# Kernel optimization log

Measured on AMD Instinct MI355X. Metric: run time of the kernel, lower is better.

Reference implementation:

```python
import jax, jax.numpy as jnp
import numpy as np

N_NODES = 10000
IN_CH = 512
HID = 128
HEADS = 4
OUT_CH = 256
N_EDGES = 160000
NEG_SLOPE = 0.2  # PyG GATConv default


def gat_conv(x, src, dst, W, a_src, a_dst, b):
    """PyG-style GATConv. x:[N,F_in], W:[F_in,H*C], a_src/a_dst:[H,C], b:[H*C].
    src/dst already include self-loops. Returns [N, H*C] (concat heads)."""
    N = x.shape[0]
    H, C = a_src.shape
    h = (x @ W).reshape(N, H, C)                     # [N,H,C]
    e_src = jnp.einsum('nhc,hc->nh', h, a_src)        # [N,H]
    e_dst = jnp.einsum('nhc,hc->nh', h, a_dst)
    alpha = jax.nn.leaky_relu(e_src[src] + e_dst[dst], NEG_SLOPE)  # [E,H]
    # softmax over incoming edges of each destination node
    m = jax.ops.segment_max(alpha, dst, num_segments=N)            # [N,H]
    ex = jnp.exp(alpha - m[dst])
    denom = jax.ops.segment_sum(ex, dst, num_segments=N)           # [N,H]
    coeff = ex / (denom[dst] + 1e-16)                              # [E,H]
    out = jax.ops.segment_sum(coeff[:, :, None] * h[src], dst, num_segments=N)  # [N,H,C]
    return out.reshape(N, H * C) + b


def _edges_with_self_loops(edge_index, n):
    loops = jnp.arange(n, dtype=edge_index.dtype)
    src = jnp.concatenate([edge_index[0], loops])
    dst = jnp.concatenate([edge_index[1], loops])
    return src, dst


def setup_inputs() -> dict:
    key = jax.random.key(0)
    ks = jax.random.split(key, 20)
    s = 0.05
    inp = {
        'x': jax.random.normal(ks[0], (N_NODES, IN_CH), jnp.float32),
        'W1': jax.random.normal(ks[1], (IN_CH, HEADS * HID), jnp.float32) * s,
        'a1s': jax.random.normal(ks[2], (HEADS, HID), jnp.float32) * s,
        'a1d': jax.random.normal(ks[3], (HEADS, HID), jnp.float32) * s,
        'b1': jnp.zeros((HEADS * HID,), jnp.float32),
        'W2': jax.random.normal(ks[4], (HEADS * HID, HEADS * HID), jnp.float32) * s,
        'a2s': jax.random.normal(ks[5], (HEADS, HID), jnp.float32) * s,
        'a2d': jax.random.normal(ks[6], (HEADS, HID), jnp.float32) * s,
        'b2': jnp.zeros((HEADS * HID,), jnp.float32),
        'W3': jax.random.normal(ks[7], (HEADS * HID, HID), jnp.float32) * s,
        'a3s': jax.random.normal(ks[8], (1, HID), jnp.float32) * s,
        'a3d': jax.random.normal(ks[9], (1, HID), jnp.float32) * s,
        'b3': jnp.zeros((HID,), jnp.float32),
        'Wl': jax.random.normal(ks[10], (HID, OUT_CH), jnp.float32) * s,
        'bl': jnp.zeros((OUT_CH,), jnp.float32),
        'Wr': jax.random.normal(ks[11], (IN_CH, OUT_CH), jnp.float32) * s,
        'br': jnp.zeros((OUT_CH,), jnp.float32),
        'edge_index': jax.random.randint(ks[12], (2, N_EDGES), 0, N_NODES, jnp.int64 if jax.config.jax_enable_x64 else jnp.int32),
    }
    return inp


def reference(x, W1, a1s, a1d, b1, W2, a2s, a2d, b2, W3, a3s, a3d, b3, Wl, bl, Wr, br, edge_index):
    src, dst = _edges_with_self_loops(edge_index, x.shape[0])
    residual = x @ Wr + br
    h = jax.nn.elu(gat_conv(x, src, dst, W1, a1s, a1d, b1))
    h = jax.nn.elu(gat_conv(h, src, dst, W2, a2s, a2d, b2))
    h = jax.nn.elu(gat_conv(h, src, dst, W3, a3s, a3d, b3))
    return h @ Wl + bl + residual
```

## Files before the change

### kernel.cpp

```cpp
#include <hip/hip_runtime.h>
#include <hip/hip_bf16.h>
#include <cstdint>
#include <cstddef>

#define N_NODES 10000
#define M_PAD   10240
#define HEADS   4

typedef __bf16 bfrag8 __attribute__((ext_vector_type(8)));
typedef __bf16 bfrag2 __attribute__((ext_vector_type(2)));
typedef float  floatx4 __attribute__((ext_vector_type(4)));
typedef float  floatx2 __attribute__((ext_vector_type(2)));

#define S0V (M_PAD * 512 / 8)
#define S1E (512 * 512 / 8)
#define S2E (512 * 512 / 8)
#define S3E (512 * 128 / 8)
#define S4E (128 * 256 / 8)
#define S5E (512 * 256 / 8)

__global__ __launch_bounds__(256) void prep(const float* __restrict__ x,
                                            const float* __restrict__ W1,
                                            const float* __restrict__ W2,
                                            const float* __restrict__ W3,
                                            const float* __restrict__ Wl,
                                            const float* __restrict__ Wr,
                                            const int* __restrict__ edst, int E,
                                            __bf16* __restrict__ xb,
                                            __bf16* __restrict__ W1T,
                                            __bf16* __restrict__ W2T,
                                            __bf16* __restrict__ W3T,
                                            __bf16* __restrict__ WlT,
                                            __bf16* __restrict__ WrT,
                                            int* __restrict__ deg) {
    int i = blockIdx.x * 256 + threadIdx.x;
    if (i < S0V) {
        int base = i * 8;
        int row = base >> 9;
        bfrag8 r = {};
        if (row < N_NODES) {
            float4 f0 = ((const float4*)x)[i * 2];
            float4 f1 = ((const float4*)x)[i * 2 + 1];
            r[0] = (__bf16)f0.x; r[1] = (__bf16)f0.y; r[2] = (__bf16)f0.z; r[3] = (__bf16)f0.w;
            r[4] = (__bf16)f1.x; r[5] = (__bf16)f1.y; r[6] = (__bf16)f1.z; r[7] = (__bf16)f1.w;
        }
        *(bfrag8*)(xb + base) = r;
    } else if ((i -= S0V) < S1E) {
        int n = i & 511, kb = (i >> 9) * 8;
        bfrag8 r;
#pragma unroll
        for (int t = 0; t < 8; ++t) r[t] = (__bf16)W1[(kb + t) * 512 + n];
        *(bfrag8*)(W1T + n * 512 + kb) = r;
    } else if ((i -= S1E) < S2E) {
        int n = i & 511, kb = (i >> 9) * 8;
        bfrag8 r;
#pragma unroll
        for (int t = 0; t < 8; ++t) r[t] = (__bf16)W2[(kb + t) * 512 + n];
        *(bfrag8*)(W2T + n * 512 + kb) = r;
    } else if ((i -= S2E) < S3E) {
        int n = i & 127, kb = (i >> 7) * 8;
        bfrag8 r;
#pragma unroll
        for (int t = 0; t < 8; ++t) r[t] = (__bf16)W3[(kb + t) * 128 + n];
        *(bfrag8*)(W3T + n * 512 + kb) = r;
    } else if ((i -= S3E) < S4E) {
        int n = i & 255, kb = (i >> 8) * 8;
        bfrag8 r;
#pragma unroll
        for (int t = 0; t < 8; ++t) r[t] = (__bf16)Wl[(kb + t) * 256 + n];
        *(bfrag8*)(WlT + n * 128 + kb) = r;
    } else if ((i -= S4E) < S5E) {
        int n = i & 255, kb = (i >> 8) * 8;
        bfrag8 r;
#pragma unroll
        for (int t = 0; t < 8; ++t) r[t] = (__bf16)Wr[(kb + t) * 256 + n];
        *(bfrag8*)(WrT + n * 512 + kb) = r;
    } else if ((i -= S5E) < E) {
        atomicAdd(&deg[edst[i]], 1);
    }
}


__global__ __launch_bounds__(1024) void scan_kernel(const int* __restrict__ deg,
                                                    int* __restrict__ rowptr,
                                                    int* __restrict__ cursor, int n) {
    __shared__ int wtot[16], woff[16];
    int t = threadIdx.x, lane = t & 63, wv = t >> 6;
    int chunk = (n + 1023) / 1024;
    int beg = t * chunk, end = beg + chunk; if (end > n) end = n; if (beg > n) beg = n;
    int s = 0;
    for (int i = beg; i < end; ++i) s += deg[i] + 1;
    int v = s;
#pragma unroll
    for (int off = 1; off < 64; off <<= 1) {
        int o = __shfl_up(v, off);
        if (lane >= off) v += o;
    }
    if (lane == 63) wtot[wv] = v;
    __syncthreads();
    if (t == 0) {
        int r = 0;
#pragma unroll
        for (int i = 0; i < 16; ++i) { woff[i] = r; r += wtot[i]; }
        rowptr[n] = r;
    }
    __syncthreads();
    int off = woff[wv] + v - s;
    for (int i = beg; i < end; ++i) {
        rowptr[i] = off; cursor[i] = off;
        off += deg[i] + 1;
    }
}

__global__ __launch_bounds__(256) void scatter_kernel(const int* __restrict__ src,
                                                      const int* __restrict__ dst, int E, int n,
                                                      int* __restrict__ cursor,
                                                      int* __restrict__ csr) {
    int i = blockIdx.x * 256 + threadIdx.x;
    if (i < E) {
        int pos = atomicAdd(&cursor[dst[i]], 1);
        csr[pos] = src[i];
    } else if (i < E + n) {
        int v = i - E;
        int pos = atomicAdd(&cursor[v], 1);
        csr[pos] = v;
    }
}


template <int NT>
__device__ __forceinline__ void gemm_loop(const __bf16* __restrict__ A,
                                          const __bf16* __restrict__ BT, int K,
                                          int m0, int n0, int wave, int lane,
                                          __bf16* As, __bf16* Bs,
                                          floatx4 (&acc)[2][NT]) {
    int r = wave * 8 + (lane >> 3);
    int kof = (lane & 7) * 8;
    const __bf16* gA = A + (size_t)(m0 + r) * K + kof;
    const __bf16* gB = BT + (size_t)(n0 + r) * K + kof;
    __bf16* lA = As + r * 64 + kof;
    __bf16* lB = Bs + r * 64 + kof;
    const __bf16* fA = As + (wave * 32 + (lane & 15)) * 64 + (lane >> 4) * 8;
    const __bf16* fB = Bs + (lane & 15) * 64 + (lane >> 4) * 8;

    for (int k0 = 0; k0 < K; k0 += 64) {
#pragma unroll
        for (int u = 0; u < 4; ++u)
            __builtin_amdgcn_global_load_lds(
                (const __attribute__((address_space(1))) void*)(gA + (size_t)u * 32 * K),
                (__attribute__((address_space(3))) void*)(lA + u * 32 * 64), 16, 0, 0);
#pragma unroll
        for (int u = 0; u < NT / 2; ++u)
            __builtin_amdgcn_global_load_lds(
                (const __attribute__((address_space(1))) void*)(gB + (size_t)u * 32 * K),
                (__attribute__((address_space(3))) void*)(lB + u * 32 * 64), 16, 0, 0);
        gA += 64; gB += 64;
        __syncthreads();

#pragma unroll
        for (int ks = 0; ks < 2; ++ks) {
            bfrag8 a0 = *(const bfrag8*)(fA + ks * 32);
            bfrag8 a1 = *(const bfrag8*)(fA + 16 * 64 + ks * 32);
#pragma unroll
            for (int nt = 0; nt < NT; ++nt) {
                bfrag8 b = *(const bfrag8*)(fB + nt * 16 * 64 + ks * 32);
                acc[0][nt] = __builtin_amdgcn_mfma_f32_16x16x32_bf16(a0, b, acc[0][nt], 0, 0, 0);
                acc[1][nt] = __builtin_amdgcn_mfma_f32_16x16x32_bf16(a1, b, acc[1][nt], 0, 0, 0);
            }
        }
        __syncthreads();
    }
}

__global__ __launch_bounds__(256) void gemm_h(const __bf16* __restrict__ A,
                                              const __bf16* __restrict__ BT,
                                              unsigned char* __restrict__ C8,
                                              int N, int K, int H,
                                              const float* __restrict__ as_,
                                              const float* __restrict__ ad_,
                                              float* __restrict__ esp,
                                              float* __restrict__ edp) {
    __shared__ __align__(16) __bf16 As[128 * 64];
    __shared__ __align__(16) __bf16 Bs[128 * 64];
    int tid = threadIdx.x, wave = tid >> 6, lane = tid & 63;
    int m0 = blockIdx.x * 128, n0 = blockIdx.y * 128;
    floatx4 acc[2][8] = {};
    gemm_loop<8>(A, BT, K, m0, n0, wave, lane, As, Bs, acc);

    int crow = m0 + wave * 32 + (lane >> 4) * 4;
    int ccol = n0 + (lane & 15);
#pragma unroll
    for (int mt = 0; mt < 2; ++mt)
#pragma unroll
        for (int nt = 0; nt < 8; ++nt)
#pragma unroll
            for (int r = 0; r < 4; ++r) {
                float v = acc[mt][nt][r];
                size_t o = (size_t)(crow + mt * 16 + r) * N + ccol + nt * 16;
                int p = __builtin_amdgcn_cvt_pk_fp8_f32(v, v, 0, false);
                C8[o] = (unsigned char)(p & 0xff);
            }

    int head = n0 >> 7;
    float a_sv[8], a_dv[8];
#pragma unroll
    for (int nt = 0; nt < 8; ++nt) {
        int cin = nt * 16 + (lane & 15);
        a_sv[nt] = as_[head * 128 + cin];
        a_dv[nt] = ad_[head * 128 + cin];
    }
#pragma unroll
    for (int mt = 0; mt < 2; ++mt)
#pragma unroll
        for (int r = 0; r < 4; ++r) {
            float ps = 0.f, pd = 0.f;
#pragma unroll
            for (int nt = 0; nt < 8; ++nt) {
                float v = acc[mt][nt][r];
                ps += v * a_sv[nt];
                pd += v * a_dv[nt];
            }
#pragma unroll
            for (int off = 8; off; off >>= 1) {
                ps += __shfl_xor(ps, off);
                pd += __shfl_xor(pd, off);
            }
            if ((lane & 15) == 0) {
                int row = crow + mt * 16 + r;
                esp[row * H + head] = ps;
                edp[row * H + head] = pd;
            }
        }
}

__global__ __launch_bounds__(256) void gemm_final(const __bf16* __restrict__ A1,
                                                  const __bf16* __restrict__ B1T, int K1,
                                                  const __bf16* __restrict__ A2,
                                                  const __bf16* __restrict__ B2T, int K2,
                                                  float* __restrict__ C,
                                                  const float* __restrict__ bias1,
                                                  const float* __restrict__ bias2,
                                                  int M, int N) {
    __shared__ __align__(16) __bf16 As[128 * 64];
    __shared__ __align__(16) __bf16 Bs[64 * 64];
    int tid = threadIdx.x, wave = tid >> 6, lane = tid & 63;
    int m0 = blockIdx.x * 128, n0 = blockIdx.y * 64;
    floatx4 acc[2][4] = {};
    gemm_loop<4>(A1, B1T, K1, m0, n0, wave, lane, As, Bs, acc);
    gemm_loop<4>(A2, B2T, K2, m0, n0, wave, lane, As, Bs, acc);

    int crow = m0 + wave * 32 + (lane >> 4) * 4;
    int ccol = n0 + (lane & 15);
#pragma unroll
    for (int mt = 0; mt < 2; ++mt)
#pragma unroll
        for (int nt = 0; nt < 4; ++nt)
#pragma unroll
            for (int r = 0; r < 4; ++r) {
                int row = crow + mt * 16 + r;
                int col = ccol + nt * 16;
                if (row < M)
                    C[(size_t)row * N + col] = acc[mt][nt][r] + bias1[col] + bias2[col];
            }
}


template <int H>
__global__ __launch_bounds__(256) void gather_agg(const unsigned char* __restrict__ H8,
                                                  const float* __restrict__ esp,
                                                  const float* __restrict__ edp,
                                                  const int* __restrict__ rowptr,
                                                  const int* __restrict__ csr,
                                                  const float* __restrict__ bias,
                                                  __bf16* __restrict__ outb) {
    constexpr int F = H * 128;
    constexpr int CH = F / 64;
    __shared__ int   sIdx[4][64];
    __shared__ float sWgt[4][64 * H];
    int wave = threadIdx.x >> 6, lane = threadIdx.x & 63;
    int node = blockIdx.x * 4 + wave;
    if (node >= M_PAD) return;
    __bf16* op = outb + (size_t)node * F + lane * CH;
    if (node >= N_NODES) {
        if (H == 4) { bfrag8 z = {}; *(bfrag8*)op = z; }
        else        { bfrag2 z = {}; *(bfrag2*)op = z; }
        return;
    }
    int hsel = (H == 4) ? (lane >> 4) : 0;
    const unsigned char* hp = H8 + lane * CH;
    int beg = rowptr[node], end = rowptr[node + 1];
    float acc[CH] = {};
    float wsum = 0.f;

    float edv0 = 0.f, edv1 = 0.f, edv2 = 0.f, edv3 = 0.f;
    if (H == 4) {
        float4 e4 = *(const float4*)(edp + node * 4);
        edv0 = e4.x; edv1 = e4.y; edv2 = e4.z; edv3 = e4.w;
    } else {
        edv0 = edp[node];
    }

    for (int t0 = beg; t0 < end; t0 += 64) {
        int n_t = end - t0; if (n_t > 64) n_t = 64;
        if (lane < n_t) {
            int s = csr[t0 + lane];
            sIdx[wave][lane] = s;
            if (H == 4) {
                float4 es = *(const float4*)(esp + s * 4);
                float tt0 = es.x + edv0; tt0 = tt0 > 0.f ? tt0 : 0.2f * tt0;
                float tt1 = es.y + edv1; tt1 = tt1 > 0.f ? tt1 : 0.2f * tt1;
                float tt2 = es.z + edv2; tt2 = tt2 > 0.f ? tt2 : 0.2f * tt2;
                float tt3 = es.w + edv3; tt3 = tt3 > 0.f ? tt3 : 0.2f * tt3;
                floatx4 w4 = { __expf(tt0), __expf(tt1), __expf(tt2), __expf(tt3) };
                *(floatx4*)&sWgt[wave][lane * 4] = w4;
            } else {
                float tt = esp[s] + edv0; tt = tt > 0.f ? tt : 0.2f * tt;
                sWgt[wave][lane] = __expf(tt);
            }
        }
        asm volatile("s_waitcnt lgkmcnt(0)" ::: "memory");

        int e = 0;
        for (; e + 3 < n_t; e += 4) {
            int s4[4]; float w4[4];
#pragma unroll
            for (int u = 0; u < 4; ++u) {
                s4[u] = sIdx[wave][e + u];
                w4[u] = sWgt[wave][(e + u) * H + hsel];
            }
            if (H == 4) {
                uint2 p4[4];
#pragma unroll
                for (int u = 0; u < 4; ++u) p4[u] = *(const uint2*)(hp + (size_t)s4[u] * F);
#pragma unroll
                for (int u = 0; u < 4; ++u) {
                    float wgt = w4[u];
                    wsum += wgt;
                    floatx2 f0 = __builtin_amdgcn_cvt_pk_f32_fp8(p4[u].x, false);
                    floatx2 f1 = __builtin_amdgcn_cvt_pk_f32_fp8(p4[u].x, true);
                    floatx2 f2 = __builtin_amdgcn_cvt_pk_f32_fp8(p4[u].y, false);
                    floatx2 f3 = __builtin_amdgcn_cvt_pk_f32_fp8(p4[u].y, true);
                    acc[0] += wgt * f0[0]; acc[1] += wgt * f0[1];
                    acc[2] += wgt * f1[0]; acc[3] += wgt * f1[1];
                    acc[4] += wgt * f2[0]; acc[5] += wgt * f2[1];
                    acc[6] += wgt * f3[0]; acc[7] += wgt * f3[1];
                }
            } else {
                unsigned short p4[4];
#pragma unroll
                for (int u = 0; u < 4; ++u) p4[u] = *(const unsigned short*)(hp + (size_t)s4[u] * F);
#pragma unroll
                for (int u = 0; u < 4; ++u) {
                    float wgt = w4[u];
                    wsum += wgt;
                    floatx2 f0 = __builtin_amdgcn_cvt_pk_f32_fp8((int)p4[u], false);
                    acc[0] += wgt * f0[0]; acc[1] += wgt * f0[1];
                }
            }
        }
        for (; e < n_t; ++e) {
            int s0 = sIdx[wave][e];
            float wgt = sWgt[wave][e * H + hsel];
            wsum += wgt;
            if (H == 4) {
                uint2 p = *(const uint2*)(hp + (size_t)s0 * F);
                floatx2 f0 = __builtin_amdgcn_cvt_pk_f32_fp8(p.x, false);
                floatx2 f1 = __builtin_amdgcn_cvt_pk_f32_fp8(p.x, true);
                floatx2 f2 = __builtin_amdgcn_cvt_pk_f32_fp8(p.y, false);
                floatx2 f3 = __builtin_amdgcn_cvt_pk_f32_fp8(p.y, true);
                acc[0] += wgt * f0[0]; acc[1] += wgt * f0[1];
                acc[2] += wgt * f1[0]; acc[3] += wgt * f1[1];
                acc[4] += wgt * f2[0]; acc[5] += wgt * f2[1];
                acc[6] += wgt * f3[0]; acc[7] += wgt * f3[1];
            } else {
                unsigned short p = *(const unsigned short*)(hp + (size_t)s0 * F);
                floatx2 f0 = __builtin_amdgcn_cvt_pk_f32_fp8((int)p, false);
                acc[0] += wgt * f0[0]; acc[1] += wgt * f0[1];
            }
        }
    }

    float inv = 1.f / (wsum + 1e-16f);
    if (H == 4) {
        bfrag8 r;
#pragma unroll
        for (int k = 0; k < 8; ++k) {
            float o = acc[k] * inv + bias[lane * 8 + k];
            o = o > 0.f ? o : __expf(o) - 1.f;
            r[k] = (__bf16)o;
        }
        *(bfrag8*)op = r;
    } else {
        bfrag2 r;
#pragma unroll
        for (int k = 0; k < 2; ++k) {
            float o = acc[k] * inv + bias[lane * 2 + k];
            o = o > 0.f ? o : __expf(o) - 1.f;
            r[k] = (__bf16)o;
        }
        *(bfrag2*)op = r;
    }
}


extern "C" void kernel_launch(void* const* d_in, const int* in_sizes, int n_in,
                              void* d_out, int out_size, void* d_ws, size_t ws_size,
                              hipStream_t stream) {
    const float* x   = (const float*)d_in[0];
    const float* W1  = (const float*)d_in[1];
    const float* a1s = (const float*)d_in[2];
    const float* a1d = (const float*)d_in[3];
    const float* b1  = (const float*)d_in[4];
    const float* W2  = (const float*)d_in[5];
    const float* a2s = (const float*)d_in[6];
    const float* a2d = (const float*)d_in[7];
    const float* b2  = (const float*)d_in[8];
    const float* W3  = (const float*)d_in[9];
    const float* a3s = (const float*)d_in[10];
    const float* a3d = (const float*)d_in[11];
    const float* b3  = (const float*)d_in[12];
    const float* Wl  = (const float*)d_in[13];
    const float* bl  = (const float*)d_in[14];
    const float* Wr  = (const float*)d_in[15];
    const float* br  = (const float*)d_in[16];
    const int*   ei  = (const int*)d_in[17];
    const int E = in_sizes[17] / 2;
    const int* esrc = ei;
    const int* edst = ei + E;
    const int slots = E + N_NODES;
    float* out = (float*)d_out;

    char* w = (char*)d_ws;
    auto alloc = [&](size_t b) { char* p = w; w += (b + 255) & ~(size_t)255; return p; };
    __bf16* xb  = (__bf16*)alloc((size_t)M_PAD * 512 * 2);
    __bf16* hb  = (__bf16*)alloc((size_t)M_PAD * 512 * 2);
    __bf16* hb3 = (__bf16*)alloc((size_t)M_PAD * 128 * 2);
    unsigned char* Hi8 = (unsigned char*)alloc((size_t)M_PAD * 512);
    __bf16* W1T = (__bf16*)alloc(512 * 512 * 2);
    __bf16* W2T = (__bf16*)alloc(512 * 512 * 2);
    __bf16* W3T = (__bf16*)alloc(128 * 512 * 2);
    __bf16* WlT = (__bf16*)alloc(256 * 128 * 2);
    __bf16* WrT = (__bf16*)alloc(256 * 512 * 2);
    float* esp    = (float*)alloc((size_t)M_PAD * HEADS * 4);
    float* edp    = (float*)alloc((size_t)M_PAD * HEADS * 4);
    int*   deg    = (int*)alloc(N_NODES * 4);
    int*   rowptr = (int*)alloc((N_NODES + 1) * 4);
    int*   cursor = (int*)alloc(N_NODES * 4);
    int*   csr    = (int*)alloc((size_t)slots * 4);

    (void)hipMemsetAsync(deg, 0, N_NODES * sizeof(int), stream);

    const int sp_total = S0V + S1E + S2E + S3E + S4E + S5E + E;
    prep<<<(sp_total + 255) / 256, 256, 0, stream>>>(x, W1, W2, W3, Wl, Wr, edst, E,
                                                     xb, W1T, W2T, W3T, WlT, WrT, deg);
    scan_kernel<<<1, 1024, 0, stream>>>(deg, rowptr, cursor, N_NODES);
    scatter_kernel<<<(E + N_NODES + 255) / 256, 256, 0, stream>>>(esrc, edst, E, N_NODES,
                                                                  cursor, csr);

    gemm_h<<<dim3(M_PAD / 128, 4), 256, 0, stream>>>(xb, W1T, Hi8, 512, 512, 4,
                                                     a1s, a1d, esp, edp);
    gather_agg<4><<<M_PAD / 4, 256, 0, stream>>>(Hi8, esp, edp, rowptr, csr, b1, hb);
    gemm_h<<<dim3(M_PAD / 128, 4), 256, 0, stream>>>(hb, W2T, Hi8, 512, 512, 4,
                                                     a2s, a2d, esp, edp);
    gather_agg<4><<<M_PAD / 4, 256, 0, stream>>>(Hi8, esp, edp, rowptr, csr, b2, hb);
    gemm_h<<<dim3(M_PAD / 128, 1), 256, 0, stream>>>(hb, W3T, Hi8, 128, 512, 1,
                                                     a3s, a3d, esp, edp);
    gather_agg<1><<<M_PAD / 4, 256, 0, stream>>>(Hi8, esp, edp, rowptr, csr, b3, hb3);
    gemm_final<<<dim3(M_PAD / 128, 4), 256, 0, stream>>>(xb, WrT, 512, hb3, WlT, 128,
                                                         out, br, bl, N_NODES, 256);
}
```

Before: 243.5 us.

## Fuse all stages into one persistent cooperative kernel with grid syncs

Replaces the separate prep, scan, scatter, GEMM, gather and final GEMM launches with a single cooperative persistent kernel of up to 320 blocks. Stages are separated by grid.sync, and the single-block scan becomes a multi-block scan. The aim is to remove launch overhead and inter-kernel gaps across about ten launches. In exchange, the GEMM and gather phases are limited to 320 resident blocks striding over tiles, which may lower occupancy and load balance. Each grid barrier also adds its own cost.

```diff
diff --git a/kernel.cpp b/kernel.cpp
--- a/kernel.cpp
+++ b/kernel.cpp
@@ -1,11 +1,15 @@
 #include <hip/hip_runtime.h>
+#include <hip/hip_cooperative_groups.h>
 #include <hip/hip_bf16.h>
 #include <cstdint>
 #include <cstddef>
 
+namespace cg = cooperative_groups;
+
 #define N_NODES 10000
 #define M_PAD   10240
 #define HEADS   4
+#define NBLK    320
 
 typedef __bf16 bfrag8 __attribute__((ext_vector_type(8)));
 typedef __bf16 bfrag2 __attribute__((ext_vector_type(2)));
@@ -19,113 +23,17 @@
 #define S4E (128 * 256 / 8)
 #define S5E (512 * 256 / 8)
 
-__global__ __launch_bounds__(256) void prep(const float* __restrict__ x,
-                                            const float* __restrict__ W1,
-                                            const float* __restrict__ W2,
-                                            const float* __restrict__ W3,
-                                            const float* __restrict__ Wl,
-                                            const float* __restrict__ Wr,
-                                            const int* __restrict__ edst, int E,
-                                            __bf16* __restrict__ xb,
-                                            __bf16* __restrict__ W1T,
-                                            __bf16* __restrict__ W2T,
-                                            __bf16* __restrict__ W3T,
-                                            __bf16* __restrict__ WlT,
-                                            __bf16* __restrict__ WrT,
-                                            int* __restrict__ deg) {
-    int i = blockIdx.x * 256 + threadIdx.x;
-    if (i < S0V) {
-        int base = i * 8;
-        int row = base >> 9;
-        bfrag8 r = {};
-        if (row < N_NODES) {
-            float4 f0 = ((const float4*)x)[i * 2];
-            float4 f1 = ((const float4*)x)[i * 2 + 1];
-            r[0] = (__bf16)f0.x; r[1] = (__bf16)f0.y; r[2] = (__bf16)f0.z; r[3] = (__bf16)f0.w;
-            r[4] = (__bf16)f1.x; r[5] = (__bf16)f1.y; r[6] = (__bf16)f1.z; r[7] = (__bf16)f1.w;
-        }
-        *(bfrag8*)(xb + base) = r;
-    } else if ((i -= S0V) < S1E) {
-        int n = i & 511, kb = (i >> 9) * 8;
-        bfrag8 r;
-#pragma unroll
-        for (int t = 0; t < 8; ++t) r[t] = (__bf16)W1[(kb + t) * 512 + n];
-        *(bfrag8*)(W1T + n * 512 + kb) = r;
-    } else if ((i -= S1E) < S2E) {
-        int n = i & 511, kb = (i >> 9) * 8;
-        bfrag8 r;
-#pragma unroll
-        for (int t = 0; t < 8; ++t) r[t] = (__bf16)W2[(kb + t) * 512 + n];
-        *(bfrag8*)(W2T + n * 512 + kb) = r;
-    } else if ((i -= S2E) < S3E) {
-        int n = i & 127, kb = (i >> 7) * 8;
-        bfrag8 r;
-#pragma unroll
-        for (int t = 0; t < 8; ++t) r[t] = (__bf16)W3[(kb + t) * 128 + n];
-        *(bfrag8*)(W3T + n * 512 + kb) = r;
-    } else if ((i -= S3E) < S4E) {
-        int n = i & 255, kb = (i >> 8) * 8;
-        bfrag8 r;
-#pragma unroll
-        for (int t = 0; t < 8; ++t) r[t] = (__bf16)Wl[(kb + t) * 256 + n];
-        *(bfrag8*)(WlT + n * 128 + kb) = r;
-    } else if ((i -= S4E) < S5E) {
-        int n = i & 255, kb = (i >> 8) * 8;
-        bfrag8 r;
-#pragma unroll
-        for (int t = 0; t < 8; ++t) r[t] = (__bf16)Wr[(kb + t) * 256 + n];
-        *(bfrag8*)(WrT + n * 512 + kb) = r;
-    } else if ((i -= S5E) < E) {
-        atomicAdd(&deg[edst[i]], 1);
-    }
-}
-
-
-__global__ __launch_bounds__(1024) void scan_kernel(const int* __restrict__ deg,
-                                                    int* __restrict__ rowptr,
-                                                    int* __restrict__ cursor, int n) {
-    __shared__ int wtot[16], woff[16];
-    int t = threadIdx.x, lane = t & 63, wv = t >> 6;
-    int chunk = (n + 1023) / 1024;
-    int beg = t * chunk, end = beg + chunk; if (end > n) end = n; if (beg > n) beg = n;
-    int s = 0;
-    for (int i = beg; i < end; ++i) s += deg[i] + 1;
-    int v = s;
-#pragma unroll
-    for (int off = 1; off < 64; off <<= 1) {
-        int o = __shfl_up(v, off);
-        if (lane >= off) v += o;
-    }
-    if (lane == 63) wtot[wv] = v;
-    __syncthreads();
-    if (t == 0) {
-        int r = 0;
-#pragma unroll
-        for (int i = 0; i < 16; ++i) { woff[i] = r; r += wtot[i]; }
-        rowptr[n] = r;
-    }
-    __syncthreads();
-    int off = woff[wv] + v - s;
-    for (int i = beg; i < end; ++i) {
-        rowptr[i] = off; cursor[i] = off;
-        off += deg[i] + 1;
-    }
-}
-
-__global__ __launch_bounds__(256) void scatter_kernel(const int* __restrict__ src,
-                                                      const int* __restrict__ dst, int E, int n,
-                                                      int* __restrict__ cursor,
-                                                      int* __restrict__ csr) {
-    int i = blockIdx.x * 256 + threadIdx.x;
-    if (i < E) {
-        int pos = atomicAdd(&cursor[dst[i]], 1);
-        csr[pos] = src[i];
-    } else if (i < E + n) {
-        int v = i - E;
-        int pos = atomicAdd(&cursor[v], 1);
-        csr[pos] = v;
-    }
-}
+struct Params {
+    const float *x, *W1, *W2, *W3, *Wl, *Wr;
+    const float *a1s, *a1d, *b1, *a2s, *a2d, *b2, *a3s, *a3d, *b3, *bl, *br;
+    const int *esrc, *edst; int E;
+    __bf16 *xb, *hb, *hb3;
+    unsigned char *Hi8;
+    __bf16 *W1T, *W2T, *W3T, *WlT, *WrT;
+    float *esp, *edp;
+    int *deg, *rowptr, *cursor, *csr, *blksum, *blkoff;
+    float *out;
+};
 
 
 template <int NT>
@@ -172,18 +80,19 @@
     }
 }
 
-__global__ __launch_bounds__(256) void gemm_h(const __bf16* __restrict__ A,
-                                              const __bf16* __restrict__ BT,
-                                              unsigned char* __restrict__ C8,
-                                              int N, int K, int H,
-                                              const float* __restrict__ as_,
-                                              const float* __restrict__ ad_,
-                                              float* __restrict__ esp,
-                                              float* __restrict__ edp) {
-    __shared__ __align__(16) __bf16 As[128 * 64];
-    __shared__ __align__(16) __bf16 Bs[128 * 64];
-    int tid = threadIdx.x, wave = tid >> 6, lane = tid & 63;
-    int m0 = blockIdx.x * 128, n0 = blockIdx.y * 128;
+__device__ __forceinline__ void gemm_h_tile(const __bf16* __restrict__ A,
+                                            const __bf16* __restrict__ BT,
+                                            unsigned char* __restrict__ C8,
+                                            int N, int K, int H,
+                                            const float* __restrict__ as_,
+                                            const float* __restrict__ ad_,
+                                            float* __restrict__ esp,
+                                            float* __restrict__ edp,
+                                            int t, char* smem, int wave, int lane) {
+    __bf16* As = (__bf16*)smem;
+    __bf16* Bs = (__bf16*)(smem + 16384);
+    int px = t % 80, py = t / 80;
+    int m0 = px * 128, n0 = py * 128;
     floatx4 acc[2][8] = {};
     gemm_loop<8>(A, BT, K, m0, n0, wave, lane, As, Bs, acc);
 
@@ -233,18 +142,19 @@
         }
 }
 
-__global__ __launch_bounds__(256) void gemm_final(const __bf16* __restrict__ A1,
-                                                  const __bf16* __restrict__ B1T, int K1,
-                                                  const __bf16* __restrict__ A2,
-                                                  const __bf16* __restrict__ B2T, int K2,
-                                                  float* __restrict__ C,
-                                                  const float* __restrict__ bias1,
-                                                  const float* __restrict__ bias2,
-                                                  int M, int N) {
-    __shared__ __align__(16) __bf16 As[128 * 64];
-    __shared__ __align__(16) __bf16 Bs[64 * 64];
-    int tid = threadIdx.x, wave = tid >> 6, lane = tid & 63;
-    int m0 = blockIdx.x * 128, n0 = blockIdx.y * 64;
+__device__ __forceinline__ void gemm_final_tile(const __bf16* __restrict__ A1,
+                                                const __bf16* __restrict__ B1T, int K1,
+                                                const __bf16* __restrict__ A2,
+                                                const __bf16* __restrict__ B2T, int K2,
+                                                float* __restrict__ C,
+                                                const float* __restrict__ bias1,
+                                                const float* __restrict__ bias2,
+                                                int M, int N,
+                                                int t, char* smem, int wave, int lane) {
+    __bf16* As = (__bf16*)smem;
+    __bf16* Bs = (__bf16*)(smem + 16384);
+    int px = t % 80, py = t / 80;
+    int m0 = px * 128, n0 = py * 64;
     floatx4 acc[2][4] = {};
     gemm_loop<4>(A1, B1T, K1, m0, n0, wave, lane, As, Bs, acc);
     gemm_loop<4>(A2, B2T, K2, m0, n0, wave, lane, As, Bs, acc);
@@ -266,20 +176,17 @@
 
 
 template <int H>
-__global__ __launch_bounds__(256) void gather_agg(const unsigned char* __restrict__ H8,
-                                                  const float* __restrict__ esp,
-                                                  const float* __restrict__ edp,
-                                                  const int* __restrict__ rowptr,
-                                                  const int* __restrict__ csr,
-                                                  const float* __restrict__ bias,
-                                                  __bf16* __restrict__ outb) {
+__device__ __forceinline__ void gather_node(const unsigned char* __restrict__ H8,
+                                            const float* __restrict__ esp,
+                                            const float* __restrict__ edp,
+                                            const int* __restrict__ rowptr,
+                                            const int* __restrict__ csr,
+                                            const float* __restrict__ bias,
+                                            __bf16* __restrict__ outb,
+                                            int node, int wave, int lane,
+                                            int* sIdx, float* sWgt) {
     constexpr int F = H * 128;
     constexpr int CH = F / 64;
-    __shared__ int   sIdx[4][64];
-    __shared__ float sWgt[4][64 * H];
-    int wave = threadIdx.x >> 6, lane = threadIdx.x & 63;
-    int node = blockIdx.x * 4 + wave;
-    if (node >= M_PAD) return;
     __bf16* op = outb + (size_t)node * F + lane * CH;
     if (node >= N_NODES) {
         if (H == 4) { bfrag8 z = {}; *(bfrag8*)op = z; }
@@ -300,11 +207,14 @@
         edv0 = edp[node];
     }
 
+    int* wIdx = sIdx + wave * 64;
+    float* wW  = sWgt + wave * 64 * H;
+
     for (int t0 = beg; t0 < end; t0 += 64) {
         int n_t = end - t0; if (n_t > 64) n_t = 64;
         if (lane < n_t) {
             int s = csr[t0 + lane];
-            sIdx[wave][lane] = s;
+            wIdx[lane] = s;
             if (H == 4) {
                 float4 es = *(const float4*)(esp + s * 4);
                 float tt0 = es.x + edv0; tt0 = tt0 > 0.f ? tt0 : 0.2f * tt0;
@@ -312,10 +222,10 @@
                 float tt2 = es.z + edv2; tt2 = tt2 > 0.f ? tt2 : 0.2f * tt2;
                 float tt3 = es.w + edv3; tt3 = tt3 > 0.f ? tt3 : 0.2f * tt3;
                 floatx4 w4 = { __expf(tt0), __expf(tt1), __expf(tt2), __expf(tt3) };
-                *(floatx4*)&sWgt[wave][lane * 4] = w4;
+                *(floatx4*)&wW[lane * 4] = w4;
             } else {
                 float tt = esp[s] + edv0; tt = tt > 0.f ? tt : 0.2f * tt;
-                sWgt[wave][lane] = __expf(tt);
+                wW[lane] = __expf(tt);
             }
         }
         asm volatile("s_waitcnt lgkmcnt(0)" ::: "memory");
@@ -325,8 +235,8 @@
             int s4[4]; float w4[4];
 #pragma unroll
             for (int u = 0; u < 4; ++u) {
-                s4[u] = sIdx[wave][e + u];
-                w4[u] = sWgt[wave][(e + u) * H + hsel];
+                s4[u] = wIdx[e + u];
+                w4[u] = wW[(e + u) * H + hsel];
             }
             if (H == 4) {
                 uint2 p4[4];
@@ -359,8 +269,8 @@
             }
         }
         for (; e < n_t; ++e) {
-            int s0 = sIdx[wave][e];
-            float wgt = sWgt[wave][e * H + hsel];
+            int s0 = wIdx[e];
+            float wgt = wW[e * H + hsel];
             wsum += wgt;
             if (H == 4) {
                 uint2 p = *(const uint2*)(hp + (size_t)s0 * F);
@@ -403,69 +313,219 @@
 }
 
 
+__global__ __launch_bounds__(256, 2) void mega(Params P) {
+    __shared__ __align__(16) char smem[32768];
+    __shared__ int wtot[4], woff[4];
+    cg::grid_group grid = cg::this_grid();
+    int tid = threadIdx.x, bid = blockIdx.x;
+    int wave = tid >> 6, lane = tid & 63;
+    int nth = gridDim.x * 256;
+    int gtid = bid * 256 + tid;
+    int* sIdx = (int*)smem;
+    float* sWgt = (float*)(smem + 4096);
+
+    {
+        int sp_total = S0V + S1E + S2E + S3E + S4E + S5E + P.E;
+        for (int it = gtid; it < sp_total; it += nth) {
+            int i = it;
+            if (i < S0V) {
+                int base = i * 8;
+                int row = base >> 9;
+                bfrag8 r = {};
+                if (row < N_NODES) {
+                    float4 f0 = ((const float4*)P.x)[i * 2];
+                    float4 f1 = ((const float4*)P.x)[i * 2 + 1];
+                    r[0] = (__bf16)f0.x; r[1] = (__bf16)f0.y; r[2] = (__bf16)f0.z; r[3] = (__bf16)f0.w;
+                    r[4] = (__bf16)f1.x; r[5] = (__bf16)f1.y; r[6] = (__bf16)f1.z; r[7] = (__bf16)f1.w;
+                }
+                *(bfrag8*)(P.xb + base) = r;
+            } else if ((i -= S0V) < S1E) {
+                int n = i & 511, kb = (i >> 9) * 8;
+                bfrag8 r;
+#pragma unroll
+                for (int t = 0; t < 8; ++t) r[t] = (__bf16)P.W1[(kb + t) * 512 + n];
+                *(bfrag8*)(P.W1T + n * 512 + kb) = r;
+            } else if ((i -= S1E) < S2E) {
+                int n = i & 511, kb = (i >> 9) * 8;
+                bfrag8 r;
+#pragma unroll
+                for (int t = 0; t < 8; ++t) r[t] = (__bf16)P.W2[(kb + t) * 512 + n];
+                *(bfrag8*)(P.W2T + n * 512 + kb) = r;
+            } else if ((i -= S2E) < S3E) {
+                int n = i & 127, kb = (i >> 7) * 8;
+                bfrag8 r;
+#pragma unroll
+                for (int t = 0; t < 8; ++t) r[t] = (__bf16)P.W3[(kb + t) * 128 + n];
+                *(bfrag8*)(P.W3T + n * 512 + kb) = r;
+            } else if ((i -= S3E) < S4E) {
+                int n = i & 255, kb = (i >> 8) * 8;
+                bfrag8 r;
+#pragma unroll
+                for (int t = 0; t < 8; ++t) r[t] = (__bf16)P.Wl[(kb + t) * 256 + n];
+                *(bfrag8*)(P.WlT + n * 128 + kb) = r;
+            } else if ((i -= S4E) < S5E) {
+                int n = i & 255, kb = (i >> 8) * 8;
+                bfrag8 r;
+#pragma unroll
+                for (int t = 0; t < 8; ++t) r[t] = (__bf16)P.Wr[(kb + t) * 256 + n];
+                *(bfrag8*)(P.WrT + n * 512 + kb) = r;
+            } else if ((i -= S5E) < P.E) {
+                atomicAdd(&P.deg[P.edst[i]], 1);
+            }
+        }
+    }
+    grid.sync();
+
+    int lex = 0, myi = 0x7fffffff;
+    if (bid < 40) {
+        int i = bid * 256 + tid; myi = i;
+        int s = (i < N_NODES) ? P.deg[i] + 1 : 0;
+        int v = s;
+#pragma unroll
+        for (int off = 1; off < 64; off <<= 1) {
+            int o = __shfl_up(v, off);
+            if (lane >= off) v += o;
+        }
+        if (lane == 63) wtot[wave] = v;
+        __syncthreads();
+        if (tid == 0) {
+            int r = 0;
+#pragma unroll
+            for (int w2 = 0; w2 < 4; ++w2) { woff[w2] = r; r += wtot[w2]; }
+            P.blksum[bid] = r;
+        }
+        __syncthreads();
+        lex = woff[wave] + v - s;
+    }
+    grid.sync();
+
+    if (bid == 0 && wave == 0) {
+        int t = (lane < 40) ? P.blksum[lane] : 0;
+        int v = t;
+#pragma unroll
+        for (int off = 1; off < 64; off <<= 1) {
+            int o = __shfl_up(v, off);
+            if (lane >= off) v += o;
+        }
+        if (lane < 40) P.blkoff[lane] = v - t;
+        if (lane == 39) P.rowptr[N_NODES] = v;
+    }
+    grid.sync();
+
+    if (myi < N_NODES) {
+        int off = P.blkoff[bid] + lex;
+        P.rowptr[myi] = off;
+        P.cursor[myi] = off;
+    }
+    grid.sync();
+
+    for (int i = gtid; i < P.E + N_NODES; i += nth) {
+        if (i < P.E) {
+            int pos = atomicAdd(&P.cursor[P.edst[i]], 1);
+            P.csr[pos] = P.esrc[i];
+        } else {
+            int v = i - P.E;
+            int pos = atomicAdd(&P.cursor[v], 1);
+            P.csr[pos] = v;
+        }
+    }
+    grid.sync();
+
+    for (int t = bid; t < 320; t += gridDim.x)
+        gemm_h_tile(P.xb, P.W1T, P.Hi8, 512, 512, 4, P.a1s, P.a1d, P.esp, P.edp,
+                    t, smem, wave, lane);
+    grid.sync();
+
+    for (int g = bid; g < M_PAD / 4; g += gridDim.x)
+        gather_node<4>(P.Hi8, P.esp, P.edp, P.rowptr, P.csr, P.b1, P.hb,
+                       g * 4 + wave, wave, lane, sIdx, sWgt);
+    grid.sync();
+
+    for (int t = bid; t < 320; t += gridDim.x)
+        gemm_h_tile(P.hb, P.W2T, P.Hi8, 512, 512, 4, P.a2s, P.a2d, P.esp, P.edp,
+                    t, smem, wave, lane);
+    grid.sync();
+
+    for (int g = bid; g < M_PAD / 4; g += gridDim.x)
+        gather_node<4>(P.Hi8, P.esp, P.edp, P.rowptr, P.csr, P.b2, P.hb,
+                       g * 4 + wave, wave, lane, sIdx, sWgt);
+    grid.sync();
+
+    for (int t = bid; t < 80; t += gridDim.x)
+        gemm_h_tile(P.hb, P.W3T, P.Hi8, 128, 512, 1, P.a3s, P.a3d, P.esp, P.edp,
+                    t, smem, wave, lane);
+    grid.sync();
+
+    for (int g = bid; g < M_PAD / 4; g += gridDim.x)
+        gather_node<1>(P.Hi8, P.esp, P.edp, P.rowptr, P.csr, P.b3, P.hb3,
+                       g * 4 + wave, wave, lane, sIdx, sWgt);
+    grid.sync();
+
+    for (int t = bid; t < 320; t += gridDim.x)
+        gemm_final_tile(P.xb, P.WrT, 512, P.hb3, P.WlT, 128, P.out, P.br, P.bl,
+                        N_NODES, 256, t, smem, wave, lane);
+}
+
+
 extern "C" void kernel_launch(void* const* d_in, const int* in_sizes, int n_in,
                               void* d_out, int out_size, void* d_ws, size_t ws_size,
                               hipStream_t stream) {
-    const float* x   = (const float*)d_in[0];
-    const float* W1  = (const float*)d_in[1];
-    const float* a1s = (const float*)d_in[2];
-    const float* a1d = (const float*)d_in[3];
-    const float* b1  = (const float*)d_in[4];
-    const float* W2  = (const float*)d_in[5];
-    const float* a2s = (const float*)d_in[6];
-    const float* a2d = (const float*)d_in[7];
-    const float* b2  = (const float*)d_in[8];
-    const float* W3  = (const float*)d_in[9];
-    const float* a3s = (const float*)d_in[10];
-    const float* a3d = (const float*)d_in[11];
-    const float* b3  = (const float*)d_in[12];
-    const float* Wl  = (const float*)d_in[13];
-    const float* bl  = (const float*)d_in[14];
-    const float* Wr  = (const float*)d_in[15];
-    const float* br  = (const float*)d_in[16];
-    const int*   ei  = (const int*)d_in[17];
-    const int E = in_sizes[17] / 2;
-    const int* esrc = ei;
-    const int* edst = ei + E;
-    const int slots = E + N_NODES;
-    float* out = (float*)d_out;
+    Params P;
+    P.x   = (const float*)d_in[0];
+    P.W1  = (const float*)d_in[1];
+    P.a1s = (const float*)d_in[2];
+    P.a1d = (const float*)d_in[3];
+    P.b1  = (const float*)d_in[4];
+    P.W2  = (const float*)d_in[5];
+    P.a2s = (const float*)d_in[6];
+    P.a2d = (const float*)d_in[7];
+    P.b2  = (const float*)d_in[8];
+    P.W3  = (const float*)d_in[9];
+    P.a3s = (const float*)d_in[10];
+    P.a3d = (const float*)d_in[11];
+    P.b3  = (const float*)d_in[12];
+    P.Wl  = (const float*)d_in[13];
+    P.bl  = (const float*)d_in[14];
+    P.Wr  = (const float*)d_in[15];
+    P.br  = (const float*)d_in[16];
+    const int* ei = (const int*)d_in[17];
+    P.E = in_sizes[17] / 2;
+    P.esrc = ei;
+    P.edst = ei + P.E;
+    const int slots = P.E + N_NODES;
+    P.out = (float*)d_out;
 
     char* w = (char*)d_ws;
     auto alloc = [&](size_t b) { char* p = w; w += (b + 255) & ~(size_t)255; return p; };
-    __bf16* xb  = (__bf16*)alloc((size_t)M_PAD * 512 * 2);
-    __bf16* hb  = (__bf16*)alloc((size_t)M_PAD * 512 * 2);
-    __bf16* hb3 = (__bf16*)alloc((size_t)M_PAD * 128 * 2);
-    unsigned char* Hi8 = (unsigned char*)alloc((size_t)M_PAD * 512);
-    __bf16* W1T = (__bf16*)alloc(512 * 512 * 2);
-    __bf16* W2T = (__bf16*)alloc(512 * 512 * 2);
-    __bf16* W3T = (__bf16*)alloc(128 * 512 * 2);
-    __bf16* WlT = (__bf16*)alloc(256 * 128 * 2);
-    __bf16* WrT = (__bf16*)alloc(256 * 512 * 2);
-    float* esp    = (float*)alloc((size_t)M_PAD * HEADS * 4);
-    float* edp    = (float*)alloc((size_t)M_PAD * HEADS * 4);
-    int*   deg    = (int*)alloc(N_NODES * 4);
-    int*   rowptr = (int*)alloc((N_NODES + 1) * 4);
-    int*   cursor = (int*)alloc(N_NODES * 4);
-    int*   csr    = (int*)alloc((size_t)slots * 4);
-
-    (void)hipMemsetAsync(deg, 0, N_NODES * sizeof(int), stream);
-
-    const int sp_total = S0V + S1E + S2E + S3E + S4E + S5E + E;
-    prep<<<(sp_total + 255) / 256, 256, 0, stream>>>(x, W1, W2, W3, Wl, Wr, edst, E,
-                                                     xb, W1T, W2T, W3T, WlT, WrT, deg);
-    scan_kernel<<<1, 1024, 0, stream>>>(deg, rowptr, cursor, N_NODES);
-    scatter_kernel<<<(E + N_NODES + 255) / 256, 256, 0, stream>>>(esrc, edst, E, N_NODES,
-                                                                  cursor, csr);
-
-    gemm_h<<<dim3(M_PAD / 128, 4), 256, 0, stream>>>(xb, W1T, Hi8, 512, 512, 4,
-                                                     a1s, a1d, esp, edp);
-    gather_agg<4><<<M_PAD / 4, 256, 0, stream>>>(Hi8, esp, edp, rowptr, csr, b1, hb);
-    gemm_h<<<dim3(M_PAD / 128, 4), 256, 0, stream>>>(hb, W2T, Hi8, 512, 512, 4,
-                                                     a2s, a2d, esp, edp);
-    gather_agg<4><<<M_PAD / 4, 256, 0, stream>>>(Hi8, esp, edp, rowptr, csr, b2, hb);
-    gemm_h<<<dim3(M_PAD / 128, 1), 256, 0, stream>>>(hb, W3T, Hi8, 128, 512, 1,
-                                                     a3s, a3d, esp, edp);
-    gather_agg<1><<<M_PAD / 4, 256, 0, stream>>>(Hi8, esp, edp, rowptr, csr, b3, hb3);
-    gemm_final<<<dim3(M_PAD / 128, 4), 256, 0, stream>>>(xb, WrT, 512, hb3, WlT, 128,
-                                                         out, br, bl, N_NODES, 256);
+    P.xb  = (__bf16*)alloc((size_t)M_PAD * 512 * 2);
+    P.hb  = (__bf16*)alloc((size_t)M_PAD * 512 * 2);
+    P.hb3 = (__bf16*)alloc((size_t)M_PAD * 128 * 2);
+    P.Hi8 = (unsigned char*)alloc((size_t)M_PAD * 512);
+    P.W1T = (__bf16*)alloc(512 * 512 * 2);
+    P.W2T = (__bf16*)alloc(512 * 512 * 2);
+    P.W3T = (__bf16*)alloc(128 * 512 * 2);
+    P.WlT = (__bf16*)alloc(256 * 128 * 2);
+    P.WrT = (__bf16*)alloc(256 * 512 * 2);
+    P.esp = (float*)alloc((size_t)M_PAD * HEADS * 4);
+    P.edp = (float*)alloc((size_t)M_PAD * HEADS * 4);
+    P.deg    = (int*)alloc(N_NODES * 4);
+    P.rowptr = (int*)alloc((N_NODES + 1) * 4);
+    P.cursor = (int*)alloc(N_NODES * 4);
+    P.csr    = (int*)alloc((size_t)slots * 4);
+    P.blksum = (int*)alloc(64 * 4);
+    P.blkoff = (int*)alloc(64 * 4);
+
+    (void)hipMemsetAsync(P.deg, 0, N_NODES * sizeof(int), stream);
+
+    int nblk = NBLK;
+    int maxb = 0;
+    if (hipOccupancyMaxActiveBlocksPerMultiprocessor(&maxb, mega, 256, 0) == hipSuccess && maxb > 0) {
+        int ncu = 0;
+        if (hipDeviceGetAttribute(&ncu, hipDeviceAttributeMultiprocessorCount, 0) == hipSuccess && ncu > 0) {
+            if (maxb * ncu < nblk) nblk = maxb * ncu;
+        }
+    }
+    void* kargs[] = { (void*)&P };
+    (void)hipLaunchCooperativeKernel((const void*)mega, dim3(nblk), dim3(256),
+                                     kargs, 0, stream);
 }
```

New measurement: 657.5 us. +170.0%, slower.

## Fuse CSR scan into prep, scatter into layer-1 GEMM, residual GEMM into layer-3 GEMM

Applied to the files above, without the earlier changes.

The degree scan now runs in the last block of the prep kernel, found through an atomic done-counter, so the separate single-block scan launch goes away. The CSR scatter runs as extra blocks of the layer-1 GEMM launch. The residual x@Wr GEMM runs alongside the small layer-3 GEMM, which on its own uses only 80 blocks and leaves the GPU underused. The final GEMM now adds onto the already-written output. Together these cut the launch count and the serialized low-occupancy phases, at the cost of a last-block tail in prep and a read-modify-write of the output.

```diff
diff --git a/kernel.cpp b/kernel.cpp
--- a/kernel.cpp
+++ b/kernel.cpp
@@ -18,6 +18,7 @@
 #define S3E (512 * 128 / 8)
 #define S4E (128 * 256 / 8)
 #define S5E (512 * 256 / 8)
+
 
 __global__ __launch_bounds__(256) void prep(const float* __restrict__ x,
                                             const float* __restrict__ W1,
@@ -32,7 +33,10 @@
                                             __bf16* __restrict__ W3T,
                                             __bf16* __restrict__ WlT,
                                             __bf16* __restrict__ WrT,
-                                            int* __restrict__ deg) {
+                                            int* __restrict__ deg,
+                                            int* __restrict__ rowptr,
+                                            int* __restrict__ cursor,
+                                            int* __restrict__ donecnt) {
     int i = blockIdx.x * 256 + threadIdx.x;
     if (i < S0V) {
         int base = i * 8;
@@ -78,18 +82,26 @@
     } else if ((i -= S5E) < E) {
         atomicAdd(&deg[edst[i]], 1);
     }
-}
-
-
-__global__ __launch_bounds__(1024) void scan_kernel(const int* __restrict__ deg,
-                                                    int* __restrict__ rowptr,
-                                                    int* __restrict__ cursor, int n) {
-    __shared__ int wtot[16], woff[16];
+
+    __threadfence();
+    __shared__ int amLast;
+    if (threadIdx.x == 0) {
+        int prev = __hip_atomic_fetch_add(donecnt, 1, __ATOMIC_ACQ_REL,
+                                          __HIP_MEMORY_SCOPE_AGENT);
+        amLast = (prev == (int)gridDim.x - 1);
+    }
+    __syncthreads();
+    if (!amLast) return;
+
+    __shared__ int wtot[4], woff[4];
     int t = threadIdx.x, lane = t & 63, wv = t >> 6;
-    int chunk = (n + 1023) / 1024;
-    int beg = t * chunk, end = beg + chunk; if (end > n) end = n; if (beg > n) beg = n;
+    const int chunk = (N_NODES + 255) / 256;
+    int beg = t * chunk, end = beg + chunk;
+    if (end > N_NODES) end = N_NODES;
+    if (beg > N_NODES) beg = N_NODES;
     int s = 0;
-    for (int i = beg; i < end; ++i) s += deg[i] + 1;
+    for (int j = beg; j < end; ++j)
+        s += __hip_atomic_load(&deg[j], __ATOMIC_RELAXED, __HIP_MEMORY_SCOPE_AGENT) + 1;
     int v = s;
 #pragma unroll
     for (int off = 1; off < 64; off <<= 1) {
@@ -101,29 +113,14 @@
     if (t == 0) {
         int r = 0;
 #pragma unroll
-        for (int i = 0; i < 16; ++i) { woff[i] = r; r += wtot[i]; }
-        rowptr[n] = r;
+        for (int w2 = 0; w2 < 4; ++w2) { woff[w2] = r; r += wtot[w2]; }
+        rowptr[N_NODES] = r;
     }
     __syncthreads();
     int off = woff[wv] + v - s;
-    for (int i = beg; i < end; ++i) {
-        rowptr[i] = off; cursor[i] = off;
-        off += deg[i] + 1;
-    }
-}
-
-__global__ __launch_bounds__(256) void scatter_kernel(const int* __restrict__ src,
-                                                      const int* __restrict__ dst, int E, int n,
-                                                      int* __restrict__ cursor,
-                                                      int* __restrict__ csr) {
-    int i = blockIdx.x * 256 + threadIdx.x;
-    if (i < E) {
-        int pos = atomicAdd(&cursor[dst[i]], 1);
-        csr[pos] = src[i];
-    } else if (i < E + n) {
-        int v = i - E;
-        int pos = atomicAdd(&cursor[v], 1);
-        csr[pos] = v;
+    for (int j = beg; j < end; ++j) {
+        rowptr[j] = off; cursor[j] = off;
+        off += __hip_atomic_load(&deg[j], __ATOMIC_RELAXED, __HIP_MEMORY_SCOPE_AGENT) + 1;
     }
 }
 
@@ -172,6 +169,66 @@
     }
 }
 
+__device__ __forceinline__ void gemm_h_tile(const __bf16* __restrict__ A,
+                                            const __bf16* __restrict__ BT,
+                                            unsigned char* __restrict__ C8,
+                                            int N, int K, int H,
+                                            const float* __restrict__ as_,
+                                            const float* __restrict__ ad_,
+                                            float* __restrict__ esp,
+                                            float* __restrict__ edp,
+                                            int t, __bf16* As, __bf16* Bs,
+                                            int wave, int lane) {
+    int m0 = (t % 80) * 128, n0 = (t / 80) * 128;
+    floatx4 acc[2][8] = {};
+    gemm_loop<8>(A, BT, K, m0, n0, wave, lane, As, Bs, acc);
+
+    int crow = m0 + wave * 32 + (lane >> 4) * 4;
+    int ccol = n0 + (lane & 15);
+#pragma unroll
+    for (int mt = 0; mt < 2; ++mt)
+#pragma unroll
+        for (int nt = 0; nt < 8; ++nt)
+#pragma unroll
+            for (int r = 0; r < 4; ++r) {
+                float v = acc[mt][nt][r];
+                size_t o = (size_t)(crow + mt * 16 + r) * N + ccol + nt * 16;
+                int p = __builtin_amdgcn_cvt_pk_fp8_f32(v, v, 0, false);
+                C8[o] = (unsigned char)(p & 0xff);
+            }
+
+    int head = n0 >> 7;
+    float a_sv[8], a_dv[8];
+#pragma unroll
+    for (int nt = 0; nt < 8; ++nt) {
+        int cin = nt * 16 + (lane & 15);
+        a_sv[nt] = as_[head * 128 + cin];
+        a_dv[nt] = ad_[head * 128 + cin];
+    }
+#pragma unroll
+    for (int mt = 0; mt < 2; ++mt)
+#pragma unroll
+        for (int r = 0; r < 4; ++r) {
+            float ps = 0.f, pd = 0.f;
+#pragma unroll
+            for (int nt = 0; nt < 8; ++nt) {
+                float v = acc[mt][nt][r];
+                ps += v * a_sv[nt];
+                pd += v * a_dv[nt];
+            }
+#pragma unroll
+            for (int off = 8; off; off >>= 1) {
+                ps += __shfl_xor(ps, off);
+                pd += __shfl_xor(pd, off);
+            }
+            if ((lane & 15) == 0) {
+                int row = crow + mt * 16 + r;
+                esp[row * H + head] = ps;
+                edp[row * H + head] = pd;
+            }
+        }
+}
+
 __global__ __launch_bounds__(256) void gemm_h(const __bf16* __restrict__ A,
                                               const __bf16* __restrict__ BT,
                                               unsigned char* __restrict__ C8,
@@ -183,71 +240,89 @@
     __shared__ __align__(16) __bf16 As[128 * 64];
     __shared__ __align__(16) __bf16 Bs[128 * 64];
     int tid = threadIdx.x, wave = tid >> 6, lane = tid & 63;
-    int m0 = blockIdx.x * 128, n0 = blockIdx.y * 128;
-    floatx4 acc[2][8] = {};
-    gemm_loop<8>(A, BT, K, m0, n0, wave, lane, As, Bs, acc);
+    int t = blockIdx.x + 80 * blockIdx.y;
+    gemm_h_tile(A, BT, C8, N, K, H, as_, ad_, esp, edp, t, As, Bs, wave, lane);
+}
+
+__global__ __launch_bounds__(256) void gemm1s(const __bf16* __restrict__ A,
+                                              const __bf16* __restrict__ BT,
+                                              unsigned char* __restrict__ C8,
+                                              const float* __restrict__ as_,
+                                              const float* __restrict__ ad_,
+                                              float* __restrict__ esp,
+                                              float* __restrict__ edp,
+                                              const int* __restrict__ esrc,
+                                              const int* __restrict__ edst, int E,
+                                              int* __restrict__ cursor,
+                                              int* __restrict__ csr) {
+    __shared__ __align__(16) __bf16 As[128 * 64];
+    __shared__ __align__(16) __bf16 Bs[128 * 64];
+    int bid = blockIdx.x;
+    if (bid >= 320) {
+        int i = (bid - 320) * 256 + threadIdx.x;
+        if (i < E) {
+            int pos = atomicAdd(&cursor[edst[i]], 1);
+            csr[pos] = esrc[i];
+        } else if (i < E + N_NODES) {
+            int v = i - E;
+            int pos = atomicAdd(&cursor[v], 1);
+            csr[pos] = v;
+        }
+        return;
+    }
+    int tid = threadIdx.x, wave = tid >> 6, lane = tid & 63;
+    gemm_h_tile(A, BT, C8, 512, 512, 4, as_, ad_, esp, edp, bid, As, Bs, wave, lane);
+}
+
+__global__ __launch_bounds__(256) void gemm3r(const __bf16* __restrict__ hb,
+                                              const __bf16* __restrict__ W3T,
+                                              unsigned char* __restrict__ C8,
+                                              const float* __restrict__ a3s,
+                                              const float* __restrict__ a3d,
+                                              float* __restrict__ esp,
+                                              float* __restrict__ edp,
+                                              const __bf16* __restrict__ xb,
+                                              const __bf16* __restrict__ WrT,
+                                              const float* __restrict__ br,
+                                              float* __restrict__ out) {
+    __shared__ __align__(16) __bf16 As[128 * 64];
+    __shared__ __align__(16) __bf16 Bs[128 * 64];
+    int tid = threadIdx.x, wave = tid >> 6, lane = tid & 63;
+    int bid = blockIdx.x;
+    if (bid < 80) {
+        gemm_h_tile(hb, W3T, C8, 128, 512, 1, a3s, a3d, esp, edp, bid, As, Bs, wave, lane);
+        return;
+    }
+    int t = bid - 80;
+    int m0 = (t % 80) * 128, n0 = (t / 80) * 64;
+    floatx4 acc[2][4] = {};
+    gemm_loop<4>(xb, WrT, 512, m0, n0, wave, lane, As, Bs, acc);
 
     int crow = m0 + wave * 32 + (lane >> 4) * 4;
     int ccol = n0 + (lane & 15);
 #pragma unroll
     for (int mt = 0; mt < 2; ++mt)
 #pragma unroll
-        for (int nt = 0; nt < 8; ++nt)
+        for (int nt = 0; nt < 4; ++nt)
 #pragma unroll
             for (int r = 0; r < 4; ++r) {
-                float v = acc[mt][nt][r];
-                size_t o = (size_t)(crow + mt * 16 + r) * N + ccol + nt * 16;
-                int p = __builtin_amdgcn_cvt_pk_fp8_f32(v, v, 0, false);
-                C8[o] = (unsigned char)(p & 0xff);
-            }
-
-    int head = n0 >> 7;
-    float a_sv[8], a_dv[8];
-#pragma unroll
-    for (int nt = 0; nt < 8; ++nt) {
-        int cin = nt * 16 + (lane & 15);
-        a_sv[nt] = as_[head * 128 + cin];
-        a_dv[nt] = ad_[head * 128 + cin];
-    }
-#pragma unroll
-    for (int mt = 0; mt < 2; ++mt)
-#pragma unroll
-        for (int r = 0; r < 4; ++r) {
-            float ps = 0.f, pd = 0.f;
-#pragma unroll
-            for (int nt = 0; nt < 8; ++nt) {
-                float v = acc[mt][nt][r];
-                ps += v * a_sv[nt];
-                pd += v * a_dv[nt];
-            }
-#pragma unroll
-            for (int off = 8; off; off >>= 1) {
-                ps += __shfl_xor(ps, off);
-                pd += __shfl_xor(pd, off);
-            }
-            if ((lane & 15) == 0) {
                 int row = crow + mt * 16 + r;
-                esp[row * H + head] = ps;
-                edp[row * H + head] = pd;
-            }
-        }
-}
-
-__global__ __launch_bounds__(256) void gemm_final(const __bf16* __restrict__ A1,
-                                                  const __bf16* __restrict__ B1T, int K1,
-                                                  const __bf16* __restrict__ A2,
-                                                  const __bf16* __restrict__ B2T, int K2,
-                                                  float* __restrict__ C,
-                                                  const float* __restrict__ bias1,
-                                                  const float* __restrict__ bias2,
-                                                  int M, int N) {
+                int col = ccol + nt * 16;
+                if (row < N_NODES)
+                    out[(size_t)row * 256 + col] = acc[mt][nt][r] + br[col];
+            }
+}
+
+__global__ __launch_bounds__(256) void gemm_acc(const __bf16* __restrict__ hb3,
+                                                const __bf16* __restrict__ WlT,
+                                                float* __restrict__ out,
+                                                const float* __restrict__ bl) {
     __shared__ __align__(16) __bf16 As[128 * 64];
     __shared__ __align__(16) __bf16 Bs[64 * 64];
     int tid = threadIdx.x, wave = tid >> 6, lane = tid & 63;
     int m0 = blockIdx.x * 128, n0 = blockIdx.y * 64;
     floatx4 acc[2][4] = {};
-    gemm_loop<4>(A1, B1T, K1, m0, n0, wave, lane, As, Bs, acc);
-    gemm_loop<4>(A2, B2T, K2, m0, n0, wave, lane, As, Bs, acc);
+    gemm_loop<4>(hb3, WlT, 128, m0, n0, wave, lane, As, Bs, acc);
 
     int crow = m0 + wave * 32 + (lane >> 4) * 4;
     int ccol = n0 + (lane & 15);
@@ -259,8 +334,10 @@
             for (int r = 0; r < 4; ++r) {
                 int row = crow + mt * 16 + r;
                 int col = ccol + nt * 16;
-                if (row < M)
-                    C[(size_t)row * N + col] = acc[mt][nt][r] + bias1[col] + bias2[col];
+                if (row < N_NODES) {
+                    size_t o = (size_t)row * 256 + col;
+                    out[o] = out[o] + acc[mt][nt][r] + bl[col];
+                }
             }
 }
 
@@ -443,29 +520,27 @@
     __bf16* WrT = (__bf16*)alloc(256 * 512 * 2);
     float* esp    = (float*)alloc((size_t)M_PAD * HEADS * 4);
     float* edp    = (float*)alloc((size_t)M_PAD * HEADS * 4);
-    int*   deg    = (int*)alloc(N_NODES * 4);
+    int*   deg    = (int*)alloc((N_NODES + 1) * 4);
     int*   rowptr = (int*)alloc((N_NODES + 1) * 4);
     int*   cursor = (int*)alloc(N_NODES * 4);
     int*   csr    = (int*)alloc((size_t)slots * 4);
 
-    (void)hipMemsetAsync(deg, 0, N_NODES * sizeof(int), stream);
+    (void)hipMemsetAsync(deg, 0, (N_NODES + 1) * sizeof(int), stream);
 
     const int sp_total = S0V + S1E + S2E + S3E + S4E + S5E + E;
     prep<<<(sp_total + 255) / 256, 256, 0, stream>>>(x, W1, W2, W3, Wl, Wr, edst, E,
-                                                     xb, W1T, W2T, W3T, WlT, WrT, deg);
-    scan_kernel<<<1, 1024, 0, stream>>>(deg, rowptr, cursor, N_NODES);
-    scatter_kernel<<<(E + N_NODES + 255) / 256, 256, 0, stream>>>(esrc, edst, E, N_NODES,
-                                                                  cursor, csr);
-
-    gemm_h<<<dim3(M_PAD / 128, 4), 256, 0, stream>>>(xb, W1T, Hi8, 512, 512, 4,
-                                                     a1s, a1d, esp, edp);
+                                                     xb, W1T, W2T, W3T, WlT, WrT,
+                                                     deg, rowptr, cursor, deg + N_NODES);
+
+    const int scat_blocks = (E + N_NODES + 255) / 256;
+    gemm1s<<<320 + scat_blocks, 256, 0, stream>>>(xb, W1T, Hi8, a1s, a1d, esp, edp,
+                                                  esrc, edst, E, cursor, csr);
     gather_agg<4><<<M_PAD / 4, 256, 0, stream>>>(Hi8, esp, edp, rowptr, csr, b1, hb);
-    gemm_h<<<dim3(M_PAD / 128, 4), 256, 0, stream>>>(hb, W2T, Hi8, 512, 512, 4,
-                                                     a2s, a2d, esp, edp);
+    gemm_h<<<dim3(80, 4), 256, 0, stream>>>(hb, W2T, Hi8, 512, 512, 4,
+                                            a2s, a2d, esp, edp);
     gather_agg<4><<<M_PAD / 4, 256, 0, stream>>>(Hi8, esp, edp, rowptr, csr, b2, hb);
-    gemm_h<<<dim3(M_PAD / 128, 1), 256, 0, stream>>>(hb, W3T, Hi8, 128, 512, 1,
-                                                     a3s, a3d, esp, edp);
+    gemm3r<<<400, 256, 0, stream>>>(hb, W3T, Hi8, a3s, a3d, esp, edp,
+                                    xb, WrT, br, out);
     gather_agg<1><<<M_PAD / 4, 256, 0, stream>>>(Hi8, esp, edp, rowptr, csr, b3, hb3);
-    gemm_final<<<dim3(M_PAD / 128, 4), 256, 0, stream>>>(xb, WrT, 512, hb3, WlT, 128,
-                                                         out, br, bl, N_NODES, 256);
-}
+    gemm_acc<<<dim3(80, 4), 256, 0, stream>>>(hb3, WlT, out, bl);
+}
```

Result: slower. 603.4 us (+147.8%).
